# Kernel optimization log

Measured on AMD Instinct MI355X. Metric: run time of the kernel, lower is better.

The kernel has to match this reference:

```python
import jax, jax.numpy as jnp
import numpy as np

K_NEIGHBORS = 10
SINKHORN_REG = 0.1
SINKHORN_ITERS = 50
EPS = 1e-10


def _pairwise_dist(x):
    # Euclidean cdist; clamp avoids sqrt(0) NaN grads on the diagonal
    sq = jnp.sum(x * x, axis=1)
    d2 = sq[:, None] + sq[None, :] - 2.0 * (x @ x.T)
    return jnp.sqrt(jnp.maximum(d2, 1e-12))


def setup_inputs() -> dict:
    key = jax.random.key(0)
    k1, k2 = jax.random.split(key)
    n, d = 8192, 128
    return {
        "embeddings": jax.random.normal(k1, (n, d), dtype=jnp.float32),
        "reference_embeddings": jax.random.normal(k2, (n, d), dtype=jnp.float32),
    }


def reference(embeddings, reference_embeddings):
    k = min(K_NEIGHBORS, embeddings.shape[0] - 1)

    cur_d = _pairwise_dist(embeddings)              # [n, n]
    ref_d = _pairwise_dist(reference_embeddings)    # [n, n]

    # k+1 smallest (ascending), drop self-distance column
    cur_knn = jnp.sort(cur_d, axis=1)[:, 1:k + 1]   # [n, k]
    ref_knn = jnp.sort(ref_d, axis=1)[:, 1:k + 1]   # [n, k]

    a = cur_knn / (jnp.sum(cur_knn, axis=1, keepdims=True) + EPS)  # [n, k]
    b = ref_knn / (jnp.sum(ref_knn, axis=1, keepdims=True) + EPS)  # [n, k]

    idx = jnp.arange(k, dtype=jnp.float32)
    M = jnp.abs(idx[None, :] - idx[:, None]) / k    # [k, k] shared cost
    Kmat = jnp.exp(-M / SINKHORN_REG)               # [k, k]

    # Batched Sinkhorn across all n samples at once
    def step(u, _):
        v = b / (u @ Kmat + EPS)          # K.T @ u per sample (K symmetric; explicit form u @ K)
        u = a / (v @ Kmat.T + EPS)        # K @ v per sample
        return u, None

    u0 = jnp.ones_like(a)
    u, _ = jax.lax.scan(step, u0, None, length=SINKHORN_ITERS)
    v = b / (u @ Kmat + EPS)

    # sum_ij u_i K_ij M_ij v_j per sample, then mean over n
    per_sample = jnp.einsum('ni,ij,nj->n', u, Kmat * M, v)
    return jnp.mean(per_sample)
```

## Files before the change

kernel.cpp:

```cpp
#include <hip/hip_runtime.h>
#include <hip/hip_bf16.h>
#include <math.h>

#define N 8192
#define D 128
#define NELEM (N * D)
#define KNN 10
#define EPSF 1e-10f
#define RT 32
#define NSLICE 16
#define RH 512
#define BIGF 3.0e38f

typedef unsigned short ushort_t;
typedef short bf16x8 __attribute__((ext_vector_type(8)));
typedef float f32x4 __attribute__((ext_vector_type(4)));

template <int L>
__device__ __forceinline__ void insM(float (&l)[L], float v) {
  #pragma unroll
  for (int q = L - 1; q >= 1; --q)
    asm("v_med3_f32 %0, %1, %2, %3"
        : "=v"(l[q]) : "v"(l[q - 1]), "v"(l[q]), "v"(v));
  asm("v_min_f32 %0, %1, %2" : "=v"(l[0]) : "v"(l[0]), "v"(v));
}

template <int L>
__device__ __forceinline__ void insP(float (&l)[L], float v) {
  #pragma unroll
  for (int q = L - 1; q >= 1; --q)
    l[q] = __builtin_amdgcn_fmed3f(l[q - 1], l[q], v);
  l[0] = fminf(l[0], v);
}

__global__ void prep_kernel(const float* __restrict__ xc,
                            const float* __restrict__ xr,
                            ushort_t* __restrict__ xb,
                            ushort_t* __restrict__ xa,
                            float* __restrict__ sq) {
  int wid  = (blockIdx.x * blockDim.x + threadIdx.x) >> 6;
  int lane = threadIdx.x & 63;
  if (wid >= 2 * N) return;
  const float* x = (wid < N) ? xc : xr;
  int row = (wid < N) ? wid : wid - N;
  float2 v = *reinterpret_cast<const float2*>(x + (size_t)row * D + lane * 2);
  float s = v.x * v.x + v.y * v.y;
  #pragma unroll
  for (int off = 32; off; off >>= 1) s += __shfl_xor(s, off, 64);
  if (lane == 0) sq[wid] = s;
  auto cvt = [](float f) -> unsigned int {
    unsigned int b = __float_as_uint(f);
    return (b + 0x7FFFu + ((b >> 16) & 1u)) >> 16;
  };
  unsigned int pb = cvt(v.x) | (cvt(v.y) << 16);
  unsigned int pa = cvt(-2.f * v.x) | (cvt(-2.f * v.y) << 16);
  *reinterpret_cast<unsigned int*>(xb + (size_t)wid * D + lane * 2) = pb;
  *reinterpret_cast<unsigned int*>(xa + (size_t)wid * D + lane * 2) = pa;
}

__global__ __launch_bounds__(256) void knn_mfma(
    const ushort_t* __restrict__ xb,
    const ushort_t* __restrict__ xa,
    const float* __restrict__ sq,
    float* __restrict__ partial) {
  __shared__ __align__(16) ushort_t Abuf[2][RT * D];
  __shared__ __align__(16) float SQs[RH];

  const int bid = blockIdx.x;
  const int mat = bid >> 10;
  const int colblk = (bid >> 4) & 63;
  const int slice = bid & 15;
  const ushort_t* __restrict__ XB = xb + (size_t)mat * NELEM;
  const ushort_t* __restrict__ XA = xa + (size_t)mat * NELEM;
  const float* __restrict__ SQ = sq + mat * N;
  const int r0 = slice * RH;
  const int t = threadIdx.x;
  const int w = t >> 6, l = t & 63;
  const int c0w = colblk * 128 + w * 32;

  if (w < 2) {
    const float* gs = SQ + r0 + w * 256 + l * 4;
    float* dsts = &SQs[w * 256];
    __builtin_amdgcn_global_load_lds(
        (const __attribute__((address_space(1))) void*)gs,
        (__attribute__((address_space(3))) void*)dsts, 16, 0, 0);
  }

  bf16x8 bfr[2][4];
  #pragma unroll
  for (int j = 0; j < 2; ++j) {
    const ushort_t* p = XB + (size_t)(c0w + j * 16 + (l & 15)) * D + (l >> 4) * 8;
    #pragma unroll
    for (int kk = 0; kk < 4; ++kk)
      bfr[j][kk] = *reinterpret_cast<const bf16x8*>(p + kk * 32);
  }

  float cand[2][KNN];
  #pragma unroll
  for (int j = 0; j < 2; ++j)
    #pragma unroll
    for (int q = 0; q < KNN; ++q) cand[j][q] = BIGF;

  const ushort_t* gbase[2];
  #pragma unroll
  for (int h = 0; h < 2; ++h) {
    const int rg = 2 * w + h;
    const int kk = rg >> 1, ii = rg & 1;
    const int row = ii * 16 + (l & 15);
    const int ch  = kk * 4 + (l >> 4);
    gbase[h] = XA + (size_t)(r0 + row) * D + ch * 8;
  }

  auto stage = [&](int tt, int bb) {
    #pragma unroll
    for (int h = 0; h < 2; ++h) {
      const ushort_t* g = gbase[h] + (size_t)tt * (RT * D);
      ushort_t* dst = &Abuf[bb][(2 * w + h) * 512];
      __builtin_amdgcn_global_load_lds(
          (const __attribute__((address_space(1))) void*)g,
          (__attribute__((address_space(3))) void*)dst, 16, 0, 0);
    }
  };

  stage(0, 0);
  asm volatile("s_waitcnt vmcnt(0)" ::: "memory");
  __syncthreads();

  for (int tt = 0; tt < RH / RT; ++tt) {
    const int cur = tt & 1;
    if (tt < RH / RT - 1) stage(tt + 1, cur ^ 1);

    f32x4 sqi[2];
    #pragma unroll
    for (int i = 0; i < 2; ++i)
      sqi[i] = *reinterpret_cast<const f32x4*>(
          &SQs[tt * RT + i * 16 + ((l >> 4) << 2)]);

    f32x4 acc[2][2];
    #pragma unroll
    for (int i = 0; i < 2; ++i)
      #pragma unroll
      for (int j = 0; j < 2; ++j) acc[i][j] = sqi[i];

    #pragma unroll
    for (int kk = 0; kk < 4; ++kk) {
      bf16x8 af[2];
      #pragma unroll
      for (int i = 0; i < 2; ++i)
        af[i] = *reinterpret_cast<const bf16x8*>(
            &Abuf[cur][(kk * 2 + i) * 512 + l * 8]);
      #pragma unroll
      for (int i = 0; i < 2; ++i)
        #pragma unroll
        for (int j = 0; j < 2; ++j)
          acc[i][j] = __builtin_amdgcn_mfma_f32_16x16x32_bf16(af[i], bfr[j][kk],
                                                              acc[i][j], 0, 0, 0);
    }

    const int rbase = r0 + tt * RT;
    const int idiff = c0w - rbase;
    if ((unsigned)(idiff + 31) < 63u) {
      #pragma unroll
      for (int i = 0; i < 2; ++i)
        #pragma unroll
        for (int j = 0; j < 2; ++j) {
          const int dd = idiff + j * 16 + (l & 15) - i * 16 - ((l >> 4) << 2);
          #pragma unroll
          for (int r = 0; r < 4; ++r)
            if (dd == r) acc[i][j][r] = BIGF;
        }
    }

    #pragma unroll
    for (int r = 0; r < 4; ++r)
      #pragma unroll
      for (int i = 0; i < 2; ++i)
        #pragma unroll
        for (int j = 0; j < 2; ++j)
          insM<KNN>(cand[j], acc[i][j][r]);

    asm volatile("s_waitcnt vmcnt(0)" ::: "memory");
    __syncthreads();
  }

  #pragma unroll
  for (int step = 16; step <= 32; step <<= 1)
    #pragma unroll
    for (int j = 0; j < 2; ++j)
      #pragma unroll
      for (int q = 0; q < KNN; ++q) {
        float o = __shfl_xor(cand[j][q], step, 64);
        insM<KNN>(cand[j], o);
      }

  if (l < 16) {
    #pragma unroll
    for (int j = 0; j < 2; ++j) {
      const int c = c0w + j * 16 + l;
      float* dst = partial + ((size_t)(mat * N + c) * NSLICE + slice) * KNN;
      #pragma unroll
      for (int q = 0; q < KNN; ++q) dst[q] = cand[j][q];
    }
  }
}

__global__ void sink_kernel(const float* __restrict__ partial,
                            const float* __restrict__ sq,
                            float* __restrict__ ps) {
  int s = blockIdx.x * blockDim.x + threadIdx.x;
  if (s >= N) return;
  constexpr float E1 = 0.36787944117144233f;

  float a[KNN], b[KNN];
  #pragma unroll
  for (int m = 0; m < 2; ++m) {
    float best[KNN];
    #pragma unroll
    for (int q = 0; q < KNN; ++q) best[q] = BIGF;
    const float* p = partial + (size_t)(m * N + s) * NSLICE * KNN;
    for (int c = 0; c < NSLICE * KNN; ++c) insP<KNN>(best, p[c]);
    const float sqc = sq[m * N + s];
    float* dst = m ? b : a;
    #pragma unroll
    for (int q = 0; q < KNN; ++q)
      dst[q] = sqrtf(fmaxf(best[q] + sqc, 1e-12f));
  }

  float suma = 0.f, sumb = 0.f;
  #pragma unroll
  for (int q = 0; q < KNN; ++q) { suma += a[q]; sumb += b[q]; }
  float rsa = __builtin_amdgcn_rcpf(suma + EPSF);
  float rsb = __builtin_amdgcn_rcpf(sumb + EPSF);
  #pragma unroll
  for (int q = 0; q < KNN; ++q) { a[q] *= rsa; b[q] *= rsb; }

  float u_[KNN], v_[KNN];
  #pragma unroll
  for (int q = 0; q < KNN; ++q) u_[q] = 1.f;

  #pragma unroll 1
  for (int it = 0; it < 50; ++it) {
    float L[KNN], S[KNN];
    L[0] = u_[0];
    #pragma unroll
    for (int q = 1; q < KNN; ++q) L[q] = fmaf(E1, L[q - 1], u_[q]);
    S[KNN - 1] = u_[KNN - 1];
    #pragma unroll
    for (int q = KNN - 2; q >= 0; --q) S[q] = fmaf(E1, S[q + 1], u_[q]);
    #pragma unroll
    for (int q = 0; q < KNN; ++q) {
      float den = (q < KNN - 1) ? fmaf(E1, S[q + 1], L[q]) : L[KNN - 1];
      v_[q] = b[q] * __builtin_amdgcn_rcpf(den + EPSF);
    }
    L[0] = v_[0];
    #pragma unroll
    for (int q = 1; q < KNN; ++q) L[q] = fmaf(E1, L[q - 1], v_[q]);
    S[KNN - 1] = v_[KNN - 1];
    #pragma unroll
    for (int q = KNN - 2; q >= 0; --q) S[q] = fmaf(E1, S[q + 1], v_[q]);
    #pragma unroll
    for (int q = 0; q < KNN; ++q) {
      float den = (q < KNN - 1) ? fmaf(E1, S[q + 1], L[q]) : L[KNN - 1];
      u_[q] = a[q] * __builtin_amdgcn_rcpf(den + EPSF);
    }
  }
  {
    float L[KNN], S[KNN];
    L[0] = u_[0];
    #pragma unroll
    for (int q = 1; q < KNN; ++q) L[q] = fmaf(E1, L[q - 1], u_[q]);
    S[KNN - 1] = u_[KNN - 1];
    #pragma unroll
    for (int q = KNN - 2; q >= 0; --q) S[q] = fmaf(E1, S[q + 1], u_[q]);
    #pragma unroll
    for (int q = 0; q < KNN; ++q) {
      float den = (q < KNN - 1) ? fmaf(E1, S[q + 1], L[q]) : L[KNN - 1];
      v_[q] = b[q] * __builtin_amdgcn_rcpf(den + EPSF);
    }
  }
  float cost = 0.f;
  #pragma unroll
  for (int i = 0; i < KNN; ++i) {
    float accr = 0.f;
    #pragma unroll
    for (int j = 0; j < KNN; ++j) {
      const int dd = i > j ? i - j : j - i;
      const float wgt = 0.1f * (float)dd * __builtin_expf(-(float)dd);
      accr = fmaf(wgt, v_[j], accr);
    }
    cost = fmaf(u_[i], accr, cost);
  }
  ps[s] = cost;
}

__global__ void reduce_kernel(const float* __restrict__ ps, float* __restrict__ out) {
  __shared__ float red[256];
  int tid = threadIdx.x;
  float s = 0.f;
  for (int i = tid; i < N; i += 256) s += ps[i];
  red[tid] = s;
  __syncthreads();
  #pragma unroll
  for (int off = 128; off > 0; off >>= 1) {
    if (tid < off) red[tid] += red[tid + off];
    __syncthreads();
  }
  if (tid == 0) out[0] = red[0] * (1.0f / N);
}

extern "C" void kernel_launch(void* const* d_in, const int* in_sizes, int n_in,
                              void* d_out, int out_size, void* d_ws, size_t ws_size,
                              hipStream_t stream) {
  const float* xc = (const float*)d_in[0];
  const float* xr = (const float*)d_in[1];
  float* out = (float*)d_out;
  char* wsb = (char*)d_ws;

  float* sq       = (float*)wsb;
  ushort_t* xb    = (ushort_t*)(wsb + (1u << 16));
  ushort_t* xa    = (ushort_t*)(wsb + (1u << 16) + (4u << 20));
  float* partial  = (float*)(wsb + (1u << 16) + (8u << 20));
  float* ps       = partial + (size_t)2 * N * NSLICE * KNN;

  prep_kernel<<<dim3(2 * N / 4), dim3(256), 0, stream>>>(xc, xr, xb, xa, sq);
  knn_mfma<<<dim3(2048), dim3(256), 0, stream>>>(xb, xa, sq, partial);
  sink_kernel<<<dim3(N / 64), dim3(64), 0, stream>>>(partial, sq, ps);
  reduce_kernel<<<dim3(1), dim3(256), 0, stream>>>(ps, out);
}
```

Baseline: 120.3 us.

## Use single-wave blocks for KNN MFMA kernel to drop block barriers

The distance/top-k kernel goes from 4-wave blocks sharing a staged row tile to single-wave blocks of 64 threads, each covering 32 columns. The row tile shrinks from 32 to 16, and the grid grows to 8192 blocks. Each wave stages its own rows into LDS and waits with a partial vmcnt instead of __syncthreads, so block barriers disappear and the prefetch overlaps compute. The cost is that each wave loads all of the A tile itself, where before four waves shared it. That means more global-to-LDS traffic per MFMA and fewer MFMAs per staged tile.

```diff
diff --git a/kernel.cpp b/kernel.cpp
--- a/kernel.cpp
+++ b/kernel.cpp
@@ -7,7 +7,7 @@
 #define NELEM (N * D)
 #define KNN 10
 #define EPSF 1e-10f
-#define RT 32
+#define RT 16
 #define NSLICE 16
 #define RH 512
 #define BIGF 3.0e38f
@@ -58,7 +58,7 @@
   *reinterpret_cast<unsigned int*>(xa + (size_t)wid * D + lane * 2) = pa;
 }
 
-__global__ __launch_bounds__(256) void knn_mfma(
+__global__ __launch_bounds__(64, 4) void knn_mfma(
     const ushort_t* __restrict__ xb,
     const ushort_t* __restrict__ xa,
     const float* __restrict__ sq,
@@ -67,20 +67,20 @@
   __shared__ __align__(16) float SQs[RH];
 
   const int bid = blockIdx.x;
-  const int mat = bid >> 10;
-  const int colblk = (bid >> 4) & 63;
+  const int mat = bid >> 12;
+  const int colgrp = (bid >> 4) & 255;
   const int slice = bid & 15;
   const ushort_t* __restrict__ XB = xb + (size_t)mat * NELEM;
   const ushort_t* __restrict__ XA = xa + (size_t)mat * NELEM;
   const float* __restrict__ SQ = sq + mat * N;
   const int r0 = slice * RH;
-  const int t = threadIdx.x;
-  const int w = t >> 6, l = t & 63;
-  const int c0w = colblk * 128 + w * 32;
-
-  if (w < 2) {
-    const float* gs = SQ + r0 + w * 256 + l * 4;
-    float* dsts = &SQs[w * 256];
+  const int l = threadIdx.x;
+  const int c0 = colgrp * 32;
+
+  #pragma unroll
+  for (int h = 0; h < 2; ++h) {
+    const float* gs = SQ + r0 + h * 256 + l * 4;
+    float* dsts = &SQs[h * 256];
     __builtin_amdgcn_global_load_lds(
         (const __attribute__((address_space(1))) void*)gs,
         (__attribute__((address_space(3))) void*)dsts, 16, 0, 0);
@@ -89,7 +89,7 @@
   bf16x8 bfr[2][4];
   #pragma unroll
   for (int j = 0; j < 2; ++j) {
-    const ushort_t* p = XB + (size_t)(c0w + j * 16 + (l & 15)) * D + (l >> 4) * 8;
+    const ushort_t* p = XB + (size_t)(c0 + j * 16 + (l & 15)) * D + (l >> 4) * 8;
     #pragma unroll
     for (int kk = 0; kk < 4; ++kk)
       bfr[j][kk] = *reinterpret_cast<const bf16x8*>(p + kk * 32);
@@ -101,21 +101,16 @@
     #pragma unroll
     for (int q = 0; q < KNN; ++q) cand[j][q] = BIGF;
 
-  const ushort_t* gbase[2];
-  #pragma unroll
-  for (int h = 0; h < 2; ++h) {
-    const int rg = 2 * w + h;
-    const int kk = rg >> 1, ii = rg & 1;
-    const int row = ii * 16 + (l & 15);
-    const int ch  = kk * 4 + (l >> 4);
-    gbase[h] = XA + (size_t)(r0 + row) * D + ch * 8;
-  }
+  const ushort_t* gbase[4];
+  #pragma unroll
+  for (int kk = 0; kk < 4; ++kk)
+    gbase[kk] = XA + (size_t)(r0 + (l & 15)) * D + (kk * 4 + (l >> 4)) * 8;
 
   auto stage = [&](int tt, int bb) {
     #pragma unroll
-    for (int h = 0; h < 2; ++h) {
-      const ushort_t* g = gbase[h] + (size_t)tt * (RT * D);
-      ushort_t* dst = &Abuf[bb][(2 * w + h) * 512];
+    for (int kk = 0; kk < 4; ++kk) {
+      const ushort_t* g = gbase[kk] + (size_t)tt * (RT * D);
+      ushort_t* dst = &Abuf[bb][kk * 512];
       __builtin_amdgcn_global_load_lds(
           (const __attribute__((address_space(1))) void*)g,
           (__attribute__((address_space(3))) void*)dst, 16, 0, 0);
@@ -124,63 +119,49 @@
 
   stage(0, 0);
   asm volatile("s_waitcnt vmcnt(0)" ::: "memory");
-  __syncthreads();
-
-  for (int tt = 0; tt < RH / RT; ++tt) {
+
+  constexpr int T = RH / RT;
+  for (int tt = 0; tt < T; ++tt) {
     const int cur = tt & 1;
-    if (tt < RH / RT - 1) stage(tt + 1, cur ^ 1);
-
-    f32x4 sqi[2];
-    #pragma unroll
-    for (int i = 0; i < 2; ++i)
-      sqi[i] = *reinterpret_cast<const f32x4*>(
-          &SQs[tt * RT + i * 16 + ((l >> 4) << 2)]);
-
-    f32x4 acc[2][2];
-    #pragma unroll
-    for (int i = 0; i < 2; ++i)
-      #pragma unroll
-      for (int j = 0; j < 2; ++j) acc[i][j] = sqi[i];
+    if (tt < T - 1) {
+      stage(tt + 1, cur ^ 1);
+      asm volatile("s_waitcnt vmcnt(4)" ::: "memory");
+    } else {
+      asm volatile("s_waitcnt vmcnt(0)" ::: "memory");
+    }
+
+    f32x4 sqi = *reinterpret_cast<const f32x4*>(&SQs[tt * RT + ((l >> 4) << 2)]);
+
+    f32x4 acc[2];
+    #pragma unroll
+    for (int j = 0; j < 2; ++j) acc[j] = sqi;
 
     #pragma unroll
     for (int kk = 0; kk < 4; ++kk) {
-      bf16x8 af[2];
-      #pragma unroll
-      for (int i = 0; i < 2; ++i)
-        af[i] = *reinterpret_cast<const bf16x8*>(
-            &Abuf[cur][(kk * 2 + i) * 512 + l * 8]);
-      #pragma unroll
-      for (int i = 0; i < 2; ++i)
+      bf16x8 af = *reinterpret_cast<const bf16x8*>(&Abuf[cur][kk * 512 + l * 8]);
+      #pragma unroll
+      for (int j = 0; j < 2; ++j)
+        acc[j] = __builtin_amdgcn_mfma_f32_16x16x32_bf16(af, bfr[j][kk],
+                                                         acc[j], 0, 0, 0);
+    }
+
+    const int rbase = r0 + tt * RT;
+    const int idiff = c0 - rbase;
+    if ((unsigned)(idiff + 31) < 47u) {
+      #pragma unroll
+      for (int j = 0; j < 2; ++j) {
+        const int dd = idiff + j * 16 + (l & 15) - ((l >> 4) << 2);
         #pragma unroll
-        for (int j = 0; j < 2; ++j)
-          acc[i][j] = __builtin_amdgcn_mfma_f32_16x16x32_bf16(af[i], bfr[j][kk],
-                                                              acc[i][j], 0, 0, 0);
-    }
-
-    const int rbase = r0 + tt * RT;
-    const int idiff = c0w - rbase;
-    if ((unsigned)(idiff + 31) < 63u) {
-      #pragma unroll
-      for (int i = 0; i < 2; ++i)
-        #pragma unroll
-        for (int j = 0; j < 2; ++j) {
-          const int dd = idiff + j * 16 + (l & 15) - i * 16 - ((l >> 4) << 2);
-          #pragma unroll
-          for (int r = 0; r < 4; ++r)
-            if (dd == r) acc[i][j][r] = BIGF;
-        }
+        for (int r = 0; r < 4; ++r)
+          if (dd == r) acc[j][r] = BIGF;
+      }
     }
 
     #pragma unroll
     for (int r = 0; r < 4; ++r)
       #pragma unroll
-      for (int i = 0; i < 2; ++i)
-        #pragma unroll
-        for (int j = 0; j < 2; ++j)
-          insM<KNN>(cand[j], acc[i][j][r]);
-
-    asm volatile("s_waitcnt vmcnt(0)" ::: "memory");
-    __syncthreads();
+      for (int j = 0; j < 2; ++j)
+        insM<KNN>(cand[j], acc[j][r]);
   }
 
   #pragma unroll
@@ -196,7 +177,7 @@
   if (l < 16) {
     #pragma unroll
     for (int j = 0; j < 2; ++j) {
-      const int c = c0w + j * 16 + l;
+      const int c = c0 + j * 16 + l;
       float* dst = partial + ((size_t)(mat * N + c) * NSLICE + slice) * KNN;
       #pragma unroll
       for (int q = 0; q < KNN; ++q) dst[q] = cand[j][q];
@@ -323,7 +304,7 @@
   float* ps       = partial + (size_t)2 * N * NSLICE * KNN;
 
   prep_kernel<<<dim3(2 * N / 4), dim3(256), 0, stream>>>(xc, xr, xb, xa, sq);
-  knn_mfma<<<dim3(2048), dim3(256), 0, stream>>>(xb, xa, sq, partial);
+  knn_mfma<<<dim3(8192), dim3(64), 0, stream>>>(xb, xa, sq, partial);
   sink_kernel<<<dim3(N / 64), dim3(64), 0, stream>>>(partial, sq, ps);
   reduce_kernel<<<dim3(1), dim3(256), 0, stream>>>(ps, out);
 }
```

After: 175.3 us. 1.46x slower.
